# Kernel tuning notes

Hardware: AMD Instinct MI355X
Metric: run time of the kernel (lower is better)

The kernel has to match this reference:

```python
import jax, jax.numpy as jnp
import numpy as np

N = 50000      # nodes
E = 800000     # edges (avg degree 32 w/ 50k nodes -> 16 per direction here)
IN = 128       # in_channels
H = 64         # hidden_channels
G = 64         # graphs in the batch
C = 2          # num_classes


def setup_inputs() -> dict:
    key = jax.random.key(0)
    ks = jax.random.split(key, 8)
    x = jax.random.normal(ks[0], (N, IN), dtype=jnp.float32)
    edge_index = jax.random.randint(ks[1], (2, E), 0, N, dtype=jnp.int64)
    batch = jnp.sort(jax.random.randint(ks[2], (N,), 0, G, dtype=jnp.int64))
    # learned parameters (glorot-ish scale)
    W1 = jax.random.normal(ks[3], (IN, H), dtype=jnp.float32) * (1.0 / np.sqrt(IN))
    b1 = jnp.zeros((H,), dtype=jnp.float32)
    W2 = jax.random.normal(ks[4], (H, H), dtype=jnp.float32) * (1.0 / np.sqrt(H))
    b2 = jnp.zeros((H,), dtype=jnp.float32)
    Wl = jax.random.normal(ks[5], (H, C), dtype=jnp.float32) * (1.0 / np.sqrt(H))
    bl = jnp.zeros((C,), dtype=jnp.float32)
    return {"x": x, "edge_index": edge_index, "batch": batch,
            "W1": W1, "b1": b1, "W2": W2, "b2": b2, "Wl": Wl, "bl": bl}


def _gcn_conv(x, src, dst, W, b, n):
    # PyG GCNConv: linear transform, add self-loops, sym-normalize, scatter-add at dst
    h = x @ W                                   # [n, H]
    loop = jnp.arange(n, dtype=src.dtype)
    s = jnp.concatenate([src, loop])            # [E+n]
    d = jnp.concatenate([dst, loop])
    deg = jax.ops.segment_sum(jnp.ones_like(d, dtype=h.dtype), d, num_segments=n)
    dinv = deg ** -0.5                          # deg >= 1 due to self-loops
    norm = dinv[s] * dinv[d]                    # [E+n]
    msg = h[s] * norm[:, None]                  # gather + scale
    out = jax.ops.segment_sum(msg, d, num_segments=n)  # scatter-add aggregate
    return out + b


def reference(x, edge_index, batch, W1, b1, W2, b2, Wl, bl):
    src, dst = edge_index[0], edge_index[1]
    h = jax.nn.relu(_gcn_conv(x, src, dst, W1, b1, N))
    # dropout is identity in eval mode
    h = jax.nn.relu(_gcn_conv(h, src, dst, W2, b2, N))
    # global mean pool per graph
    counts = jax.ops.segment_sum(jnp.ones((N,), dtype=h.dtype), batch, num_segments=G)
    pooled = jax.ops.segment_sum(h, batch, num_segments=G) / jnp.maximum(counts, 1.0)[:, None]
    out = pooled @ Wl + bl                      # [G, C]
    return (out, pooled)
```

## Files before the change

### kernel.cpp

```cpp
#include <hip/hip_runtime.h>

#define N_NODES   50000
#define N_EDGES   800000
#define IN_CH     128
#define HID       64
#define N_GRAPHS  64
#define N_CLASSES 2
#define NBLK_SCAN ((N_NODES + 255) / 256)


__global__ void deg_kernel(const int* __restrict__ ei, int* __restrict__ degCount) {
    int e = blockIdx.x * blockDim.x + threadIdx.x;
    if (e < N_EDGES) {
        int dst = ei[N_EDGES + e];
        atomicAdd(&degCount[dst], 1);
    }
}

__global__ __launch_bounds__(256) void scan1_kernel(const int* __restrict__ degCount,
                                                    int* __restrict__ blockSums) {
    __shared__ int red[256];
    int i = blockIdx.x * 256 + threadIdx.x;
    red[threadIdx.x] = (i < N_NODES) ? degCount[i] : 0;
    __syncthreads();
    for (int off = 128; off > 0; off >>= 1) {
        if (threadIdx.x < off) red[threadIdx.x] += red[threadIdx.x + off];
        __syncthreads();
    }
    if (threadIdx.x == 0) blockSums[blockIdx.x] = red[0];
}

__global__ __launch_bounds__(256) void scan2_kernel(int* __restrict__ blockSums) {
    __shared__ int s[256];
    int t = threadIdx.x;
    int v = (t < NBLK_SCAN) ? blockSums[t] : 0;
    s[t] = v;
    __syncthreads();
    for (int off = 1; off < 256; off <<= 1) {
        int a = (t >= off) ? s[t - off] : 0;
        __syncthreads();
        s[t] += a;
        __syncthreads();
    }
    if (t < NBLK_SCAN) blockSums[t] = s[t] - v;
}

__global__ __launch_bounds__(256) void scan3_kernel(int* __restrict__ degFill,
                                                    const int* __restrict__ blockSums,
                                                    int* __restrict__ rowPtr,
                                                    float* __restrict__ dinv) {
    __shared__ int s[256];
    int t = threadIdx.x;
    int i = blockIdx.x * 256 + t;
    int d = (i < N_NODES) ? degFill[i] : 0;
    s[t] = d;
    __syncthreads();
    for (int off = 1; off < 256; off <<= 1) {
        int a = (t >= off) ? s[t - off] : 0;
        __syncthreads();
        s[t] += a;
        __syncthreads();
    }
    int excl = s[t] - d + blockSums[blockIdx.x];
    if (i < N_NODES) {
        rowPtr[i]  = excl;
        degFill[i] = excl;
        dinv[i]    = 1.0f / sqrtf((float)(d + 1));
    }
    if (i == 0) rowPtr[N_NODES] = N_EDGES;
}

__global__ void fill_kernel(const int* __restrict__ ei,
                            int* __restrict__ fillPtr, int* __restrict__ colIdx) {
    int e = blockIdx.x * blockDim.x + threadIdx.x;
    if (e < N_EDGES) {
        int src = ei[e];
        int dst = ei[N_EDGES + e];
        int pos = atomicAdd(&fillPtr[dst], 1);
        colIdx[pos] = src;
    }
}

#define FMA4(xs, w, a) { (a).x = fmaf((xs), (w).x, (a).x); \
                         (a).y = fmaf((xs), (w).y, (a).y); \
                         (a).z = fmaf((xs), (w).z, (a).z); \
                         (a).w = fmaf((xs), (w).w, (a).w); }

template <int K>
__global__ __launch_bounds__(256) void gemm_kernel(const float* __restrict__ A,
                                                   const float* __restrict__ W,
                                                   const float* __restrict__ dinv,
                                                   float* __restrict__ out) {
    __shared__ float4 Ws[K * 16];
    for (int i = threadIdx.x; i < K * 16; i += 256)
        Ws[i] = ((const float4*)W)[i];
    __syncthreads();

    const int c4   = threadIdx.x & 15;
    const int rg   = threadIdx.x >> 4;
    const int row0 = blockIdx.x * 128 + rg * 8;

    const float4* ap[8];
#pragma unroll
    for (int r = 0; r < 8; ++r) {
        int rowc = min(row0 + r, N_NODES - 1);
        ap[r] = (const float4*)(A + (size_t)rowc * K);
    }

    float4 acc[8] = {};
    for (int kk = 0; kk < K / 4; ++kk) {
        float4 xv[8];
#pragma unroll
        for (int r = 0; r < 8; ++r) xv[r] = ap[r][kk];
        float4 w;
        w = Ws[(4 * kk + 0) * 16 + c4];
#pragma unroll
        for (int r = 0; r < 8; ++r) FMA4(xv[r].x, w, acc[r]);
        w = Ws[(4 * kk + 1) * 16 + c4];
#pragma unroll
        for (int r = 0; r < 8; ++r) FMA4(xv[r].y, w, acc[r]);
        w = Ws[(4 * kk + 2) * 16 + c4];
#pragma unroll
        for (int r = 0; r < 8; ++r) FMA4(xv[r].z, w, acc[r]);
        w = Ws[(4 * kk + 3) * 16 + c4];
#pragma unroll
        for (int r = 0; r < 8; ++r) FMA4(xv[r].w, w, acc[r]);
    }

#pragma unroll
    for (int r = 0; r < 8; ++r) {
        int row = row0 + r;
        if (row < N_NODES) {
            float dv = dinv[row];
            float4 o = acc[r];
            o.x *= dv; o.y *= dv; o.z *= dv; o.w *= dv;
            ((float4*)(out + (size_t)row * HID))[c4] = o;
        }
    }
}

__global__ __launch_bounds__(256) void agg_kernel(const float* __restrict__ g,
                                                  const float* __restrict__ dinv,
                                                  const int* __restrict__ rowPtr,
                                                  const int* __restrict__ colIdx,
                                                  const float* __restrict__ bias,
                                                  float* __restrict__ out) {
    int lane = threadIdx.x & 63;
    int v = blockIdx.x * 4 + (threadIdx.x >> 6);
    if (v >= N_NODES) return;

    float acc = g[(size_t)v * HID + lane];
    int e  = rowPtr[v];
    int e1 = rowPtr[v + 1];
    for (; e + 3 < e1; e += 4) {
        int u0 = colIdx[e], u1 = colIdx[e + 1], u2 = colIdx[e + 2], u3 = colIdx[e + 3];
        float a0 = g[(size_t)u0 * HID + lane];
        float a1 = g[(size_t)u1 * HID + lane];
        float a2 = g[(size_t)u2 * HID + lane];
        float a3 = g[(size_t)u3 * HID + lane];
        acc += (a0 + a1) + (a2 + a3);
    }
    for (; e < e1; ++e) acc += g[(size_t)colIdx[e] * HID + lane];

    float r = dinv[v] * acc + bias[lane];
    out[(size_t)v * HID + lane] = fmaxf(r, 0.f);
}

__global__ __launch_bounds__(256) void pool_kernel(const float* __restrict__ h,
                                                   const int* __restrict__ batch,
                                                   const float* __restrict__ Wl,
                                                   const float* __restrict__ bl,
                                                   float* __restrict__ dout) {
    __shared__ int bounds[2];
    __shared__ float red[4][64];
    int g = blockIdx.x;
    if (threadIdx.x < 2) {
        int target = g + (int)threadIdx.x;
        int lo = 0, hi = N_NODES;
        while (lo < hi) {
            int mid = (lo + hi) >> 1;
            if (batch[mid] < target) lo = mid + 1; else hi = mid;
        }
        bounds[threadIdx.x] = lo;
    }
    __syncthreads();
    int start = bounds[0], end = bounds[1];
    int lane = threadIdx.x & 63, w = threadIdx.x >> 6;

    float acc = 0.f;
    for (int r = start + w; r < end; r += 4)
        acc += h[(size_t)r * HID + lane];
    red[w][lane] = acc;
    __syncthreads();
    if (w == 0) {
        float s = red[0][lane] + red[1][lane] + red[2][lane] + red[3][lane];
        float cnt = (float)(end - start);
        float p = s / fmaxf(cnt, 1.0f);
        dout[N_GRAPHS * N_CLASSES + g * HID + lane] = p;
        red[0][lane] = p;
    }
    __syncthreads();
    if (threadIdx.x < N_CLASSES) {
        float o = bl[threadIdx.x];
        for (int k = 0; k < HID; ++k)
            o = fmaf(red[0][k], Wl[k * N_CLASSES + threadIdx.x], o);
        dout[g * N_CLASSES + threadIdx.x] = o;
    }
}

extern "C" void kernel_launch(void* const* d_in, const int* in_sizes, int n_in,
                              void* d_out, int out_size, void* d_ws, size_t ws_size,
                              hipStream_t stream) {
    const float* x     = (const float*)d_in[0];
    const int*   ei    = (const int*)d_in[1];
    const int*   batch = (const int*)d_in[2];
    const float* W1    = (const float*)d_in[3];
    const float* b1    = (const float*)d_in[4];
    const float* W2    = (const float*)d_in[5];
    const float* b2    = (const float*)d_in[6];
    const float* Wl    = (const float*)d_in[7];
    const float* bl    = (const float*)d_in[8];
    float* out = (float*)d_out;

    char* ws = (char*)d_ws;
    size_t off = 0;
    auto alloc = [&](size_t bytes) -> void* {
        void* p = ws + off;
        off += (bytes + 255) & ~(size_t)255;
        return p;
    };
    int*   degFill   = (int*)  alloc((size_t)N_NODES * 4);
    int*   rowPtr    = (int*)  alloc((size_t)(N_NODES + 1) * 4);
    float* dinv      = (float*)alloc((size_t)N_NODES * 4);
    int*   blockSums = (int*)  alloc((size_t)NBLK_SCAN * 4);
    int*   colIdx    = (int*)  alloc((size_t)N_EDGES * 4);
    float* bufA      = (float*)alloc((size_t)N_NODES * HID * 4);
    float* bufB      = (float*)alloc((size_t)N_NODES * HID * 4);

    hipMemsetAsync(degFill, 0, (size_t)N_NODES * 4, stream);

    deg_kernel  <<<(N_EDGES + 255) / 256, 256, 0, stream>>>(ei, degFill);
    scan1_kernel<<<NBLK_SCAN, 256, 0, stream>>>(degFill, blockSums);
    scan2_kernel<<<1, 256, 0, stream>>>(blockSums);
    scan3_kernel<<<NBLK_SCAN, 256, 0, stream>>>(degFill, blockSums, rowPtr, dinv);
    fill_kernel <<<(N_EDGES + 255) / 256, 256, 0, stream>>>(ei, degFill, colIdx);

    gemm_kernel<IN_CH><<<(N_NODES + 127) / 128, 256, 0, stream>>>(x, W1, dinv, bufA);
    agg_kernel        <<<N_NODES / 4, 256, 0, stream>>>(bufA, dinv, rowPtr, colIdx, b1, bufB);

    gemm_kernel<HID>  <<<(N_NODES + 127) / 128, 256, 0, stream>>>(bufB, W2, dinv, bufA);
    agg_kernel        <<<N_NODES / 4, 256, 0, stream>>>(bufA, dinv, rowPtr, colIdx, b2, bufB);

    pool_kernel<<<N_GRAPHS, 256, 0, stream>>>(bufB, batch, Wl, bl, out);
}
```

Before: 348.3 us.

## Split mean pooling into parallel atomic partial sums plus finalize kernel

Replaces the one-block-per-graph pooling kernel, which read about 780 rows per block over only 64 blocks, with a kernel that spreads rows across about 196 blocks. Each wave accumulates runs of consecutive rows that share a graph id and flushes them with atomicAdd into a small pooled-sum buffer. A second tiny kernel divides by the per-graph counts and applies the final linear layer with wave shuffles. This is meant to fix the poor parallelism of the pooling stage, at the cost of an extra memset, an extra launch and float atomics whose summation order is not deterministic.

```diff
diff --git a/kernel.cpp b/kernel.cpp
--- a/kernel.cpp
+++ b/kernel.cpp
@@ -166,45 +166,56 @@
     out[(size_t)v * HID + lane] = fmaxf(r, 0.f);
 }
 
-__global__ __launch_bounds__(256) void pool_kernel(const float* __restrict__ h,
+__global__ __launch_bounds__(256) void pool1_kernel(const float* __restrict__ h,
+                                                    const int* __restrict__ batch,
+                                                    float* __restrict__ pooledSum) {
+    int lane = threadIdx.x & 63;
+    int w    = threadIdx.x >> 6;
+    int base = blockIdx.x * 256 + w;
+
+    float acc = 0.f;
+    int curg = -1;
+    for (int k = 0; k < 64; ++k) {
+        int row = base + k * 4;
+        if (row >= N_NODES) break;
+        int g = batch[row];
+        if (g != curg) {
+            if (curg >= 0) atomicAdd(&pooledSum[curg * HID + lane], acc);
+            acc = 0.f;
+            curg = g;
+        }
+        acc += h[(size_t)row * HID + lane];
+    }
+    if (curg >= 0) atomicAdd(&pooledSum[curg * HID + lane], acc);
+}
+
+__global__ __launch_bounds__(64) void pool2_kernel(const float* __restrict__ pooledSum,
                                                    const int* __restrict__ batch,
                                                    const float* __restrict__ Wl,
                                                    const float* __restrict__ bl,
                                                    float* __restrict__ dout) {
-    __shared__ int bounds[2];
-    __shared__ float red[4][64];
-    int g = blockIdx.x;
-    if (threadIdx.x < 2) {
-        int target = g + (int)threadIdx.x;
-        int lo = 0, hi = N_NODES;
-        while (lo < hi) {
-            int mid = (lo + hi) >> 1;
-            if (batch[mid] < target) lo = mid + 1; else hi = mid;
-        }
-        bounds[threadIdx.x] = lo;
-    }
-    __syncthreads();
-    int start = bounds[0], end = bounds[1];
-    int lane = threadIdx.x & 63, w = threadIdx.x >> 6;
-
-    float acc = 0.f;
-    for (int r = start + w; r < end; r += 4)
-        acc += h[(size_t)r * HID + lane];
-    red[w][lane] = acc;
-    __syncthreads();
-    if (w == 0) {
-        float s = red[0][lane] + red[1][lane] + red[2][lane] + red[3][lane];
-        float cnt = (float)(end - start);
-        float p = s / fmaxf(cnt, 1.0f);
-        dout[N_GRAPHS * N_CLASSES + g * HID + lane] = p;
-        red[0][lane] = p;
-    }
-    __syncthreads();
-    if (threadIdx.x < N_CLASSES) {
-        float o = bl[threadIdx.x];
-        for (int k = 0; k < HID; ++k)
-            o = fmaf(red[0][k], Wl[k * N_CLASSES + threadIdx.x], o);
-        dout[g * N_CLASSES + threadIdx.x] = o;
+    int g    = blockIdx.x;
+    int lane = threadIdx.x;
+
+    int lo0 = 0, hi = N_NODES;
+    while (lo0 < hi) { int mid = (lo0 + hi) >> 1; if (batch[mid] < g) lo0 = mid + 1; else hi = mid; }
+    int lo1 = lo0; hi = N_NODES;
+    while (lo1 < hi) { int mid = (lo1 + hi) >> 1; if (batch[mid] < g + 1) lo1 = mid + 1; else hi = mid; }
+    float cnt = (float)(lo1 - lo0);
+
+    float p = pooledSum[g * HID + lane] / fmaxf(cnt, 1.0f);
+    dout[N_GRAPHS * N_CLASSES + g * HID + lane] = p;
+
+    float p0 = p * Wl[lane * N_CLASSES + 0];
+    float p1 = p * Wl[lane * N_CLASSES + 1];
+#pragma unroll
+    for (int off = 32; off > 0; off >>= 1) {
+        p0 += __shfl_down(p0, off, 64);
+        p1 += __shfl_down(p1, off, 64);
+    }
+    if (lane == 0) {
+        dout[g * N_CLASSES + 0] = p0 + bl[0];
+        dout[g * N_CLASSES + 1] = p1 + bl[1];
     }
 }
 
@@ -233,11 +244,13 @@
     int*   rowPtr    = (int*)  alloc((size_t)(N_NODES + 1) * 4);
     float* dinv      = (float*)alloc((size_t)N_NODES * 4);
     int*   blockSums = (int*)  alloc((size_t)NBLK_SCAN * 4);
+    float* pooledSum = (float*)alloc((size_t)N_GRAPHS * HID * 4);
     int*   colIdx    = (int*)  alloc((size_t)N_EDGES * 4);
     float* bufA      = (float*)alloc((size_t)N_NODES * HID * 4);
     float* bufB      = (float*)alloc((size_t)N_NODES * HID * 4);
 
     hipMemsetAsync(degFill, 0, (size_t)N_NODES * 4, stream);
+    hipMemsetAsync(pooledSum, 0, (size_t)N_GRAPHS * HID * 4, stream);
 
     deg_kernel  <<<(N_EDGES + 255) / 256, 256, 0, stream>>>(ei, degFill);
     scan1_kernel<<<NBLK_SCAN, 256, 0, stream>>>(degFill, blockSums);
@@ -251,5 +264,6 @@
     gemm_kernel<HID>  <<<(N_NODES + 127) / 128, 256, 0, stream>>>(bufB, W2, dinv, bufA);
     agg_kernel        <<<N_NODES / 4, 256, 0, stream>>>(bufA, dinv, rowPtr, colIdx, b2, bufB);
 
-    pool_kernel<<<N_GRAPHS, 256, 0, stream>>>(bufB, batch, Wl, bl, out);
-}
+    pool1_kernel<<<NBLK_SCAN, 256, 0, stream>>>(bufB, batch, pooledSum);
+    pool2_kernel<<<N_GRAPHS, 64, 0, stream>>>(pooledSum, batch, Wl, bl, out);
+}
```

Measured after the change: 333.0 us. 4.4% less time.
